# Optimization experiments

Hardware: AMD Instinct MI355X
Metric: run time of the kernel (lower is better)

## Reference

```python
import jax, jax.numpy as jnp
import numpy as np

N_NODES = 4096
N_EDGES = 131072
N_GRAPHS = 16
F_IN = 128
NUM_CLASSES = 10
NH = 4  # heads per MHA and number of MHA modules
D = 128  # embed dim after conv2
HD = D // NH  # 32 per-head dim


def setup_inputs() -> dict:
    key = jax.random.key(0)
    ks = jax.random.split(key, 20)
    p = lambda i, shape: jax.random.normal(ks[i], shape, dtype=jnp.float32) * 0.05
    return {
        "x": jax.random.normal(ks[0], (N_NODES, F_IN), dtype=jnp.float32),
        "edge_index": jax.random.randint(ks[1], (2, N_EDGES), 0, N_NODES, dtype=jnp.int32),
        "batch": jnp.sort(jax.random.randint(ks[2], (N_NODES,), 0, N_GRAPHS, dtype=jnp.int32)),
        # GCN layers (PyG GCNConv: lin without bias, bias added after aggregation)
        "W1": p(3, (64, F_IN)), "b1": p(4, (64,)),
        "W2": p(5, (128, 64)), "b2": p(6, (128,)),
        # 4 MultiheadAttention modules, params stacked on axis 0
        "W_in": p(7, (NH, 3 * D, D)), "b_in": p(8, (NH, 3 * D)),
        "W_out": p(9, (NH, D, D)), "b_out": p(10, (NH, D)),
        # MLP head
        "Wf1": p(11, (256, D * NH)), "bf1": p(12, (256,)),
        "Wf2": p(13, (NUM_CLASSES, 256)), "bf2": p(14, (NUM_CLASSES,)),
    }


def gcn_conv(x, src, dst, dinv, W, b):
    # x' = x @ W.T; out[i] = sum_{j->i} dinv[j]*dinv[i] * x'[j] + b  (self-loops in src/dst)
    h = x @ W.T
    norm = dinv[src] * dinv[dst]  # [E+N]
    msg = h[src] * norm[:, None]
    return jax.ops.segment_sum(msg, dst, num_segments=N_NODES) + b


def mha(x, W_in, b_in, W_out, b_out):
    # x: [N, D] treated as batch=1, seq=N (torch MHA self-attention)
    qkv = x @ W_in.T + b_in  # [N, 3D]
    q, k, v = jnp.split(qkv, 3, axis=-1)
    q = q.reshape(-1, NH, HD).transpose(1, 0, 2)  # [H, N, HD]
    k = k.reshape(-1, NH, HD).transpose(1, 0, 2)
    v = v.reshape(-1, NH, HD).transpose(1, 0, 2)
    scores = jnp.einsum("hnd,hmd->hnm", q, k) / jnp.sqrt(jnp.float32(HD))
    attn = jax.nn.softmax(scores, axis=-1)
    o = jnp.einsum("hnm,hmd->hnd", attn, v)  # [H, N, HD]
    o = o.transpose(1, 0, 2).reshape(-1, D)  # [N, D]
    return o @ W_out.T + b_out


def reference(x, edge_index, batch, W1, b1, W2, b2, W_in, b_in, W_out, b_out, Wf1, bf1, Wf2, bf2):
    # add self-loops (PyG GCNConv default)
    loop = jnp.arange(N_NODES, dtype=edge_index.dtype)
    src = jnp.concatenate([edge_index[0], loop])
    dst = jnp.concatenate([edge_index[1], loop])
    deg = jax.ops.segment_sum(jnp.ones_like(src, dtype=jnp.float32), dst, num_segments=N_NODES)
    dinv = jnp.where(deg > 0, jax.lax.rsqrt(jnp.maximum(deg, 1.0)), 0.0)

    h = jax.nn.relu(gcn_conv(x, src, dst, dinv, W1, b1))
    h = jax.nn.relu(gcn_conv(h, src, dst, dinv, W2, b2))

    # 4 independent MHA modules over the same node sequence, concatenated
    outs = jax.vmap(mha, in_axes=(None, 0, 0, 0, 0))(h, W_in, b_in, W_out, b_out)  # [4, N, D]
    h = outs.transpose(1, 0, 2).reshape(N_NODES, D * NH)  # [N, 512]

    # global mean pool per graph
    sums = jax.ops.segment_sum(h, batch, num_segments=N_GRAPHS)
    cnts = jax.ops.segment_sum(jnp.ones((N_NODES,), jnp.float32), batch, num_segments=N_GRAPHS)
    g = sums / jnp.maximum(cnts, 1.0)[:, None]  # [16, 512]

    g = jax.nn.relu(g @ Wf1.T + bf1)
    logits = g @ Wf2.T + bf2
    return jax.nn.log_softmax(logits, axis=1)
```

## Files before the change

### kernel.cpp

```cpp
#include <hip/hip_runtime.h>
#include <hip/hip_bf16.h>

#define N_NODES 4096
#define N_EDGES 131072
#define N_GRAPHS 16
#define F_IN 128
#define D 128
#define QKVLD 1536
#define KSPL 2
#define CHUNK 64
#define NT (2048 / CHUNK)

typedef __hip_bfloat16 bf16;
typedef __attribute__((ext_vector_type(4))) float f32x4;
typedef __attribute__((ext_vector_type(8))) short bf16x8;

__device__ __forceinline__ short f2bf(float f) {
    unsigned u = __float_as_uint(f);
    unsigned r = (u + 0x7fffu + ((u >> 16) & 1u)) >> 16;
    return (short)r;
}
__device__ __forceinline__ float bf2f(short b) {
    return __uint_as_float(((unsigned)(unsigned short)b) << 16);
}
__device__ __forceinline__ float ldf(const void* p, long i, int isbf) {
    return isbf ? bf2f(((const short*)p)[i]) : ((const float*)p)[i];
}
__device__ __forceinline__ int swzK(int a) { return a ^ (((a >> 7) & 3) << 4); }
__device__ __forceinline__ int swzV(int a) { return a ^ (((a >> 7) & 7) << 4); }

__global__ void k_detect(const void* __restrict__ x, int* __restrict__ flag) {
    if (threadIdx.x == 0 && blockIdx.x == 0) {
        const unsigned short* h = (const unsigned short*)x;
        int bf = 1;
        for (int i = 0; i < 64; ++i) {
            int e = (h[i] >> 7) & 0xFF;
            if (e >= 134) { bf = 0; break; }
        }
        *flag = bf;
    }
}

struct ConvSegs {
    const void* src0; const void* src1; const void* src2; const void* src3; const void* src4;
    short* dst0; short* dst1; short* dst2; short* dst3; short* dst4;
    int e0, e1, e2, e3, e4;
};
__global__ void k_tobf16(ConvSegs s, const int* __restrict__ flag) {
    int idx = blockIdx.x * 256 + threadIdx.x;
    int isbf = *flag;
    const void* src; short* dst; int base;
    if (idx < s.e0)      { src = s.src0; dst = s.dst0; base = 0; }
    else if (idx < s.e1) { src = s.src1; dst = s.dst1; base = s.e0; }
    else if (idx < s.e2) { src = s.src2; dst = s.dst2; base = s.e1; }
    else if (idx < s.e3) { src = s.src3; dst = s.dst3; base = s.e2; }
    else if (idx < s.e4) { src = s.src4; dst = s.dst4; base = s.e3; }
    else return;
    int i = idx - base;
    dst[i] = f2bf(ldf(src, i, isbf));
}

__global__ void k_deg(const int* __restrict__ dst, int* __restrict__ degi) {
    int e = blockIdx.x * 256 + threadIdx.x;
    if (e < N_EDGES) atomicAdd(&degi[dst[e]], 1);
}

__global__ __launch_bounds__(1024) void k_prep(const int* __restrict__ degi,
                                               const int* __restrict__ batch,
                                               int* __restrict__ offs,
                                               int* __restrict__ cursor,
                                               float* __restrict__ dinv,
                                               int* __restrict__ starts) {
    __shared__ int part[1024];
    int t = threadIdx.x;
    int4 v = *(const int4*)(degi + t * 4);
    int dv[4] = {v.x, v.y, v.z, v.w};
    int s = dv[0] + dv[1] + dv[2] + dv[3];
    part[t] = s;
    __syncthreads();
    for (int ofs = 1; ofs < 1024; ofs <<= 1) {
        int val = (t >= ofs) ? part[t - ofs] : 0;
        __syncthreads();
        part[t] += val;
        __syncthreads();
    }
    int o = part[t] - s;
#pragma unroll
    for (int j = 0; j < 4; ++j) {
        int n = t * 4 + j;
        offs[n] = o; cursor[n] = o;
        o += dv[j];
        dinv[n] = rsqrtf((float)(dv[j] + 1));
    }
    if (t == 1023) offs[4096] = o;
#pragma unroll
    for (int j = 0; j < 4; ++j) {
        int n = t * 4 + j;
        int b = batch[n];
        if (n == 0) { for (int g2 = 0; g2 <= b; ++g2) starts[g2] = 0; }
        else {
            int pb = batch[n - 1];
            for (int g2 = pb + 1; g2 <= b; ++g2) starts[g2] = n;
        }
        if (n == N_NODES - 1) { for (int g2 = b + 1; g2 <= N_GRAPHS; ++g2) starts[g2] = N_NODES; }
    }
}

__global__ void k_sortedges(const int* __restrict__ src, const int* __restrict__ dst,
                            int* __restrict__ cursor, int* __restrict__ sSrc) {
    int e = blockIdx.x * 256 + threadIdx.x;
    if (e >= N_EDGES) return;
    int d = dst[e];
    int pos = atomicAdd(&cursor[d], 1);
    sSrc[pos] = src[e];
}

__global__ __launch_bounds__(64) void k_mfma_gemm_s(const short* __restrict__ A, int lda,
                                                    const short* __restrict__ W,
                                                    short* __restrict__ C, int ldc, int K) {
    const int lane = threadIdx.x;
    const int m15 = lane & 15, quad = lane >> 4;
    const int c0 = blockIdx.x * 16;
    const int n0 = blockIdx.y * 16;
    f32x4 acc = {0.f, 0.f, 0.f, 0.f};
    for (int k0 = 0; k0 < K; k0 += 32) {
        bf16x8 a = *(const bf16x8*)(A + (long)(n0 + m15) * lda + k0 + quad * 8);
        bf16x8 b = *(const bf16x8*)(W + (long)(c0 + m15) * K + k0 + quad * 8);
        acc = __builtin_amdgcn_mfma_f32_16x16x32_bf16(a, b, acc, 0, 0, 0);
    }
#pragma unroll
    for (int i = 0; i < 4; ++i)
        C[(long)(n0 + quad * 4 + i) * ldc + c0 + m15] = f2bf(acc[i]);
}

__global__ __launch_bounds__(64) void k_qkv(const short* __restrict__ h2b,
                                            const short* __restrict__ Winb,
                                            const void* __restrict__ bin,
                                            const int* __restrict__ flag,
                                            short* __restrict__ Qb,
                                            short* __restrict__ Kb,
                                            short* __restrict__ VTb) {
    const int lane = threadIdx.x;
    const int m15 = lane & 15, quad = lane >> 4;
    const int c0 = blockIdx.x * 16;
    const int n0 = blockIdx.y * 16;
    f32x4 acc = {0.f, 0.f, 0.f, 0.f};
#pragma unroll
    for (int k0 = 0; k0 < 128; k0 += 32) {
        bf16x8 a = *(const bf16x8*)(h2b + (long)(n0 + m15) * 128 + k0 + quad * 8);
        bf16x8 b = *(const bf16x8*)(Winb + (long)(c0 + m15) * 128 + k0 + quad * 8);
        acc = __builtin_amdgcn_mfma_f32_16x16x32_bf16(a, b, acc, 0, 0, 0);
    }
    const int c = c0 + m15;
    const int mmod = c / 384;
    const int r = c - mmod * 384;
    const int sect = r >> 7;
    const int rr = r & 127;
    const int head = mmod * 4 + (rr >> 5);
    const int d = rr & 31;
    const float bias = ldf(bin, c, *flag);
    if (sect == 0) {
        const float scale = 0.17677669529663687f * 1.4426950408889634f;
#pragma unroll
        for (int i = 0; i < 4; ++i)
            Qb[(long)head * 131072 + (long)(n0 + quad * 4 + i) * 32 + d] = f2bf((acc[i] + bias) * scale);
    } else if (sect == 1) {
#pragma unroll
        for (int i = 0; i < 4; ++i)
            Kb[(long)head * 131072 + (long)(n0 + quad * 4 + i) * 32 + d] = f2bf(acc[i] + bias);
    } else {
        long vbase = (long)head * 131072 + (long)d * 4096;
#pragma unroll
        for (int i = 0; i < 4; ++i) {
            int n = n0 + quad * 4 + i;
            int phys = (n & ~31) | ((((n >> 2) & 3) << 3) | (((n >> 4) & 1) << 2) | (n & 3));
            VTb[vbase + phys] = f2bf(acc[i] + bias);
        }
    }
}

__global__ __launch_bounds__(64) void k_gather64(const short* __restrict__ hlin,
                                                 const int* __restrict__ offs,
                                                 const int* __restrict__ sSrc,
                                                 const float* __restrict__ dinv,
                                                 const void* __restrict__ bias,
                                                 const int* __restrict__ flag,
                                                 short* __restrict__ houtb) {
    int n = blockIdx.x;
    int c = threadIdx.x;
    int beg = offs[n], end = offs[n + 1];
    float di = dinv[n];
    float acc = 0.f;
    for (int j = beg; j < end; ++j) {
        int s = sSrc[j];
        acc += dinv[s] * bf2f(hlin[(long)s * 64 + c]);
    }
    float v = fmaxf(di * acc + di * di * bf2f(hlin[(long)n * 64 + c]) + ldf(bias, c, *flag), 0.f);
    houtb[(long)n * 64 + c] = f2bf(v);
}

__global__ __launch_bounds__(128) void k_gather128(const short* __restrict__ hlin,
                                                   const int* __restrict__ offs,
                                                   const int* __restrict__ sSrc,
                                                   const float* __restrict__ dinv,
                                                   const void* __restrict__ bias,
                                                   const int* __restrict__ flag,
                                                   short* __restrict__ h2b) {
    int n = blockIdx.x;
    int c = threadIdx.x;
    int beg = offs[n], end = offs[n + 1];
    float di = dinv[n];
    float acc = 0.f;
    for (int j = beg; j < end; ++j) {
        int s = sSrc[j];
        acc += dinv[s] * bf2f(hlin[(long)s * 128 + c]);
    }
    float v = fmaxf(di * acc + di * di * bf2f(hlin[(long)n * 128 + c]) + ldf(bias, c, *flag), 0.f);
    h2b[(long)n * 128 + c] = f2bf(v);
}

__global__ __launch_bounds__(512) void k_attn_v13(const short* __restrict__ Qb,
                                                  const short* __restrict__ Kb,
                                                  const short* __restrict__ VTb,
                                                  short* __restrict__ po_base,
                                                  float* __restrict__ pl) {
    const int tid = threadIdx.x;
    const int lane = tid & 63;
    const int wid = tid >> 6;
    const int m15 = lane & 15, quad = lane >> 4;
    const int b = blockIdx.x;
    const int mh = (b & 7) + 8 * (b >> 8);
    const int mid = (b >> 3) & 31;
    const int z = mid & 1;
    const int qb = mid >> 1;
    const int q0 = qb * 256 + wid * 32;
    const long hoff = (long)mh * 131072;
    const short* Qh = Qb + hoff;
    const short* Kh = Kb + hoff;
    const short* Vh = VTb + hoff;
    const int ks0 = z * 2048;

    __shared__ short Klds[2][2048];
    __shared__ short Vlds[2][2048];

    int myOff, dstB;
    if (tid < 256) {
        int r = tid >> 2, part = tid & 3;
        myOff = r * 32 + part * 8;
        dstB  = swzK(r * 64 + part * 16);
    } else {
        int u = tid - 256;
        int d = u >> 3, part = u & 7;
        myOff = d * 4096 + part * 8;
        dstB  = swzV(d * 128 + part * 16);
    }

    const bf16x8 qf0 = *(const bf16x8*)(Qh + (long)(q0 + m15) * 32 + quad * 8);
    const bf16x8 qf1 = *(const bf16x8*)(Qh + (long)(q0 + 16 + m15) * 32 + quad * 8);

    const int k00 = swzK((0 * 32 + m15) * 64 + quad * 16);
    const int k01 = swzK((0 * 32 + 16 + m15) * 64 + quad * 16);
    const int k10 = swzK((1 * 32 + m15) * 64 + quad * 16);
    const int k11 = swzK((1 * 32 + 16 + m15) * 64 + quad * 16);
    const int v00 = swzV(m15 * 128 + 0 * 64 + quad * 16);
    const int v01 = swzV((16 + m15) * 128 + 0 * 64 + quad * 16);
    const int v10 = swzV(m15 * 128 + 1 * 64 + quad * 16);
    const int v11 = swzV((16 + m15) * 128 + 1 * 64 + quad * 16);

    f32x4 oA0 = {0.f,0.f,0.f,0.f}, oA1 = {0.f,0.f,0.f,0.f};
    f32x4 oB0 = {0.f,0.f,0.f,0.f}, oB1 = {0.f,0.f,0.f,0.f};
    float lq0 = 0.f, lq1 = 0.f;

    int4 nx = (tid < 256) ? *(const int4*)(Kh + (long)ks0 * 32 + myOff)
                          : *(const int4*)(Vh + myOff + ks0);
    if (tid < 256) *(int4*)((char*)&Klds[0][0] + dstB) = nx;
    else           *(int4*)((char*)&Vlds[0][0] + dstB) = nx;
    __syncthreads();

    int cur = 0;
    for (int c = 0; c < NT; ++c) {
        const bool more = (c + 1 < NT);
        if (more) {
            int kc = ks0 + (c + 1) * CHUNK;
            nx = (tid < 256) ? *(const int4*)(Kh + (long)kc * 32 + myOff)
                             : *(const int4*)(Vh + myOff + kc);
        }
        const char* Kc = (const char*)&Klds[cur][0];
        const char* Vc = (const char*)&Vlds[cur][0];
#pragma unroll
        for (int s = 0; s < 2; ++s) {
            bf16x8 kf0 = *(const bf16x8*)(Kc + (s ? k10 : k00));
            bf16x8 kf1 = *(const bf16x8*)(Kc + (s ? k11 : k01));
            bf16x8 vf0 = *(const bf16x8*)(Vc + (s ? v10 : v00));
            bf16x8 vf1 = *(const bf16x8*)(Vc + (s ? v11 : v01));
            const f32x4 zz = {0.f,0.f,0.f,0.f};
            __builtin_amdgcn_s_setprio(1);
            f32x4 sA0 = __builtin_amdgcn_mfma_f32_16x16x32_bf16(kf0, qf0, zz, 0, 0, 0);
            f32x4 sA1 = __builtin_amdgcn_mfma_f32_16x16x32_bf16(kf1, qf0, zz, 0, 0, 0);
            f32x4 sB0 = __builtin_amdgcn_mfma_f32_16x16x32_bf16(kf0, qf1, zz, 0, 0, 0);
            f32x4 sB1 = __builtin_amdgcn_mfma_f32_16x16x32_bf16(kf1, qf1, zz, 0, 0, 0);
            __builtin_amdgcn_s_setprio(0);
            float pA0[4], pA1[4], pB0[4], pB1[4];
#pragma unroll
            for (int i = 0; i < 4; ++i) {
                pA0[i] = __builtin_amdgcn_exp2f(fminf(sA0[i], 100.f));
                pA1[i] = __builtin_amdgcn_exp2f(fminf(sA1[i], 100.f));
                pB0[i] = __builtin_amdgcn_exp2f(fminf(sB0[i], 100.f));
                pB1[i] = __builtin_amdgcn_exp2f(fminf(sB1[i], 100.f));
            }
            lq0 += (pA0[0] + pA0[1]) + (pA0[2] + pA0[3]) + (pA1[0] + pA1[1]) + (pA1[2] + pA1[3]);
            lq1 += (pB0[0] + pB0[1]) + (pB0[2] + pB0[3]) + (pB1[0] + pB1[1]) + (pB1[2] + pB1[3]);
            union { unsigned u[4]; bf16x8 v; } aq0, aq1;
            aq0.u[0] = __builtin_amdgcn_perm(__float_as_uint(pA0[1]), __float_as_uint(pA0[0]), 0x07060302u);
            aq0.u[1] = __builtin_amdgcn_perm(__float_as_uint(pA0[3]), __float_as_uint(pA0[2]), 0x07060302u);
            aq0.u[2] = __builtin_amdgcn_perm(__float_as_uint(pA1[1]), __float_as_uint(pA1[0]), 0x07060302u);
            aq0.u[3] = __builtin_amdgcn_perm(__float_as_uint(pA1[3]), __float_as_uint(pA1[2]), 0x07060302u);
            aq1.u[0] = __builtin_amdgcn_perm(__float_as_uint(pB0[1]), __float_as_uint(pB0[0]), 0x07060302u);
            aq1.u[1] = __builtin_amdgcn_perm(__float_as_uint(pB0[3]), __float_as_uint(pB0[2]), 0x07060302u);
            aq1.u[2] = __builtin_amdgcn_perm(__float_as_uint(pB1[1]), __float_as_uint(pB1[0]), 0x07060302u);
            aq1.u[3] = __builtin_amdgcn_perm(__float_as_uint(pB1[3]), __float_as_uint(pB1[2]), 0x07060302u);
            __builtin_amdgcn_s_setprio(1);
            oA0 = __builtin_amdgcn_mfma_f32_16x16x32_bf16(aq0.v, vf0, oA0, 0, 0, 0);
            oA1 = __builtin_amdgcn_mfma_f32_16x16x32_bf16(aq0.v, vf1, oA1, 0, 0, 0);
            oB0 = __builtin_amdgcn_mfma_f32_16x16x32_bf16(aq1.v, vf0, oB0, 0, 0, 0);
            oB1 = __builtin_amdgcn_mfma_f32_16x16x32_bf16(aq1.v, vf1, oB1, 0, 0, 0);
            __builtin_amdgcn_s_setprio(0);
        }
        if (more) {
            if (tid < 256) *(int4*)((char*)&Klds[cur ^ 1][0] + dstB) = nx;
            else           *(int4*)((char*)&Vlds[cur ^ 1][0] + dstB) = nx;
        }
        __syncthreads();
        cur ^= 1;
    }

    lq0 += __shfl_xor(lq0, 16); lq0 += __shfl_xor(lq0, 32);
    lq1 += __shfl_xor(lq1, 16); lq1 += __shfl_xor(lq1, 32);

    short* po = po_base + (long)z * 2097152;
    const int base = (mh >> 2) * 128 + (mh & 3) * 32;
#pragma unroll
    for (int i = 0; i < 4; ++i) {
        int qa = q0 + quad * 4 + i;
        int qb2 = qa + 16;
        po[(long)qa * 512 + base + m15]       = f2bf(oA0[i]);
        po[(long)qa * 512 + base + 16 + m15]  = f2bf(oA1[i]);
        po[(long)qb2 * 512 + base + m15]      = f2bf(oB0[i]);
        po[(long)qb2 * 512 + base + 16 + m15] = f2bf(oB1[i]);
    }
    if (quad == 0) {
        pl[z * 65536 + mh * 4096 + q0 + m15] = lq0;
        pl[z * 65536 + mh * 4096 + q0 + 16 + m15] = lq1;
    }
}

__global__ __launch_bounds__(64) void k_outproj(const short* __restrict__ po,
                                                const float* __restrict__ pl,
                                                const short* __restrict__ Woutb,
                                                const void* __restrict__ bout,
                                                const int* __restrict__ flag,
                                                float* __restrict__ hcat) {
    const int lane = threadIdx.x;
    const int m15 = lane & 15, quad = lane >> 4;
    const int c0 = blockIdx.x * 16;
    const int n0 = blockIdx.y * 16;
    const int m = blockIdx.z;
    const int n = n0 + m15;
    f32x4 acc = {0.f,0.f,0.f,0.f};
#pragma unroll
    for (int k0 = 0; k0 < 128; k0 += 32) {
        const int head = m * 4 + (k0 >> 5);
        float l = pl[head * 4096 + n] + pl[65536 + head * 4096 + n];
        float inv = 1.f / fmaxf(l, 1e-30f);
        long base = (long)n * 512 + m * 128 + k0 + quad * 8;
        bf16x8 a0 = *(const bf16x8*)(po + base);
        bf16x8 a1 = *(const bf16x8*)(po + 2097152 + base);
        bf16x8 av;
#pragma unroll
        for (int j = 0; j < 8; ++j)
            av[j] = f2bf((bf2f(a0[j]) + bf2f(a1[j])) * inv);
        bf16x8 bv = *(const bf16x8*)(Woutb + (long)(m * 128 + c0 + m15) * 128 + k0 + quad * 8);
        acc = __builtin_amdgcn_mfma_f32_16x16x32_bf16(av, bv, acc, 0, 0, 0);
    }
    float bias = ldf(bout, m * 128 + c0 + m15, *flag);
#pragma unroll
    for (int i = 0; i < 4; ++i)
        hcat[(long)(n0 + quad * 4 + i) * 512 + m * 128 + c0 + m15] = acc[i] + bias;
}

__global__ __launch_bounds__(1024) void k_pool3(const float* __restrict__ hcat,
                                                const int* __restrict__ starts,
                                                float* __restrict__ g) {
    int gr = blockIdx.x, cg = blockIdx.y;
    int tx = threadIdx.x, ty = threadIdx.y;
    int c = cg * 128 + tx;
    int beg = starts[gr], end = starts[gr + 1];
    float s = 0.f;
    for (int n = beg + ty; n < end; n += 8)
        s += hcat[(long)n * 512 + c];
    __shared__ float red[8][128];
    red[ty][tx] = s;
    __syncthreads();
    if (ty == 0) {
        float t = ((red[0][tx] + red[1][tx]) + (red[2][tx] + red[3][tx]))
                + ((red[4][tx] + red[5][tx]) + (red[6][tx] + red[7][tx]));
        int cnt = end - beg;
        g[gr * 512 + c] = t / (float)(cnt > 0 ? cnt : 1);
    }
}

__global__ void k_gemm_mlp(const float* __restrict__ A, int lda,
                           const void* __restrict__ W,
                           const void* __restrict__ bias,
                           const int* __restrict__ flag,
                           float* __restrict__ C, int ldc,
                           int M, int N, int K, int relu) {
    const int wb = *flag;
    __shared__ float As[16][17];
    __shared__ float Ws[16][17];
    int tx = threadIdx.x, ty = threadIdx.y;
    int row = blockIdx.y * 16 + ty;
    int col = blockIdx.x * 16 + tx;
    float acc = 0.f;
    for (int k0 = 0; k0 < K; k0 += 16) {
        As[ty][tx] = (row < M && (k0 + tx) < K) ? A[(long)row * lda + k0 + tx] : 0.f;
        int wrow = blockIdx.x * 16 + ty;
        Ws[ty][tx] = (wrow < N && (k0 + tx) < K) ? ldf(W, (long)wrow * K + k0 + tx, wb) : 0.f;
        __syncthreads();
#pragma unroll
        for (int kk = 0; kk < 16; ++kk) acc += As[ty][kk] * Ws[tx][kk];
        __syncthreads();
    }
    if (row < M && col < N) {
        if (bias) acc += ldf(bias, col, wb);
        if (relu) acc = fmaxf(acc, 0.f);
        C[(long)row * ldc + col] = acc;
    }
}

__global__ void k_logsoftmax(const float* __restrict__ logits, const int* __restrict__ flag,
                             void* __restrict__ out) {
    int t = threadIdx.x;
    if (t >= N_GRAPHS) return;
    int isbf = *flag;
    float v[10];
    float mx = -1e30f;
    for (int c = 0; c < 10; ++c) { v[c] = logits[t * 10 + c]; mx = fmaxf(mx, v[c]); }
    float s = 0.f;
    for (int c = 0; c < 10; ++c) s += __expf(v[c] - mx);
    float lse = mx + __logf(s);
    for (int c = 0; c < 10; ++c) {
        float r = v[c] - lse;
        if (isbf) ((bf16*)out)[t * 10 + c] = (bf16)r;
        else      ((float*)out)[t * 10 + c] = r;
    }
}

extern "C" void kernel_launch(void* const* d_in, const int* in_sizes, int n_in,
                              void* d_out, int out_size, void* d_ws, size_t ws_size,
                              hipStream_t stream) {
    const void* x     = d_in[0];
    const int*  ei    = (const int*)d_in[1];
    const int*  batch = (const int*)d_in[2];
    const void* W1    = d_in[3];
    const void* b1    = d_in[4];
    const void* W2    = d_in[5];
    const void* b2    = d_in[6];
    const void* W_in  = d_in[7];
    const void* b_in  = d_in[8];
    const void* W_out = d_in[9];
    const void* b_out = d_in[10];
    const void* Wf1   = d_in[11];
    const void* bf1   = d_in[12];
    const void* Wf2   = d_in[13];
    const void* bf2   = d_in[14];

    const int* src = ei;
    const int* dst = ei + N_EDGES;

    float* w = (float*)d_ws;
    size_t off = 0;
    auto alloc = [&](size_t n) { float* p = w + off; off += (n + 63) & ~(size_t)63; return p; };
    int*   flag   = (int*)alloc(64);
    float* dinv   = alloc(N_NODES);
    float* g      = alloc(N_GRAPHS * 512);
    float* hid    = alloc(N_GRAPHS * 256);
    float* logits = alloc(N_GRAPHS * 10);
    int*   degi   = (int*)alloc(N_NODES);
    int*   offs   = (int*)alloc(N_NODES + 64);
    int*   cursor = (int*)alloc(N_NODES);
    int*   sSrc   = (int*)alloc(N_EDGES);
    int*   starts = (int*)alloc(64);
    float* pl     = alloc(KSPL * 16 * N_NODES);
    float* xbf    = alloc(262144);
    float* W1bf   = alloc(4096);
    float* W2bf   = alloc(4096);
    float* Winbf  = alloc(98304);
    float* Woutbf = alloc(32768);
    float* h1linbf= alloc(131072);
    float* h2linbf= alloc(262144);
    float* h1bf   = alloc(131072);
    float* h2bf   = alloc(262144);
    float* pobf   = alloc((size_t)KSPL * 1048576);
    float* hcat   = alloc(2097152);
    float* bufQ   = alloc(3145728);

    short* xb    = (short*)xbf;
    short* W1b   = (short*)W1bf;
    short* W2b   = (short*)W2bf;
    short* Winb  = (short*)Winbf;
    short* Woutb = (short*)Woutbf;
    short* h1lin = (short*)h1linbf;
    short* h2lin = (short*)h2linbf;
    short* h1b   = (short*)h1bf;
    short* h2b   = (short*)h2bf;
    short* po    = (short*)pobf;
    short* Qb    = (short*)bufQ;
    short* Kb    = Qb + 2097152;
    short* VTb   = Qb + 4194304;

    dim3 b256(256);

    k_detect<<<dim3(1), dim3(64), 0, stream>>>(x, flag);

    ConvSegs cs;
    cs.src0 = x;     cs.dst0 = xb;    cs.e0 = 524288;
    cs.src1 = W1;    cs.dst1 = W1b;   cs.e1 = cs.e0 + 8192;
    cs.src2 = W2;    cs.dst2 = W2b;   cs.e2 = cs.e1 + 8192;
    cs.src3 = W_in;  cs.dst3 = Winb;  cs.e3 = cs.e2 + 196608;
    cs.src4 = W_out; cs.dst4 = Woutb; cs.e4 = cs.e3 + 65536;
    k_tobf16<<<dim3((802816 + 255) / 256), b256, 0, stream>>>(cs, flag);

    hipMemsetAsync(degi, 0, N_NODES * sizeof(int), stream);
    k_deg<<<dim3((N_EDGES + 255) / 256), b256, 0, stream>>>(dst, degi);
    k_prep<<<dim3(1), dim3(1024), 0, stream>>>(degi, batch, offs, cursor, dinv, starts);
    k_sortedges<<<dim3((N_EDGES + 255) / 256), b256, 0, stream>>>(src, dst, cursor, sSrc);

    k_mfma_gemm_s<<<dim3(4, N_NODES / 16), dim3(64), 0, stream>>>(
        xb, F_IN, W1b, h1lin, 64, F_IN);
    k_gather64<<<dim3(N_NODES), dim3(64), 0, stream>>>(h1lin, offs, sSrc, dinv, b1, flag, h1b);

    k_mfma_gemm_s<<<dim3(8, N_NODES / 16), dim3(64), 0, stream>>>(
        h1b, 64, W2b, h2lin, 128, 64);
    k_gather128<<<dim3(N_NODES), dim3(128), 0, stream>>>(h2lin, offs, sSrc, dinv, b2, flag, h2b);

    k_qkv<<<dim3(96, N_NODES / 16), dim3(64), 0, stream>>>(
        h2b, Winb, b_in, flag, Qb, Kb, VTb);

    k_attn_v13<<<dim3(512), dim3(512), 0, stream>>>(Qb, Kb, VTb, po, pl);

    k_outproj<<<dim3(8, N_NODES / 16, 4), dim3(64), 0, stream>>>(
        po, pl, Woutb, b_out, flag, hcat);

    k_pool3<<<dim3(N_GRAPHS, 4), dim3(128, 8), 0, stream>>>(hcat, starts, g);
    k_gemm_mlp<<<dim3(256 / 16, 1), dim3(16, 16), 0, stream>>>(
        g, 512, Wf1, bf1, flag, hid, 256, N_GRAPHS, 256, 512, 1);
    k_gemm_mlp<<<dim3(1, 1), dim3(16, 16), 0, stream>>>(
        hid, 256, Wf2, bf2, flag, logits, 10, N_GRAPHS, 10, 256, 0);
    k_logsoftmax<<<dim3(1), dim3(64), 0, stream>>>(logits, flag, d_out);
}
```

Baseline: 293.2 us.

## Double attention K/V chunk size and split normalization out of out-projection

The attention kernel now stages 128-key chunks of K and V in shared memory instead of 64, so every thread loads both a K and a V vector each step, and the V swizzle is adjusted for the wider row stride. This halves the number of barrier-separated iterations and spreads the load work across all threads, at the cost of twice the LDS footprint per block. The softmax-denominator normalization and the merge of the two key-split partials move out of the out-projection GEMM into a separate k_norm kernel. The out-projection previously redid that work for every column tile; the new kernel does it once, but adds a launch and an extra write and read of the normalized buffer.

```diff
diff --git a/kernel.cpp b/kernel.cpp
--- a/kernel.cpp
+++ b/kernel.cpp
@@ -8,7 +8,7 @@
 #define D 128
 #define QKVLD 1536
 #define KSPL 2
-#define CHUNK 64
+#define CHUNK 128
 #define NT (2048 / CHUNK)
 
 typedef __hip_bfloat16 bf16;
@@ -27,7 +27,7 @@
     return isbf ? bf2f(((const short*)p)[i]) : ((const float*)p)[i];
 }
 __device__ __forceinline__ int swzK(int a) { return a ^ (((a >> 7) & 3) << 4); }
-__device__ __forceinline__ int swzV(int a) { return a ^ (((a >> 7) & 7) << 4); }
+__device__ __forceinline__ int swzV(int a) { return a ^ (((a >> 8) & 7) << 4); }
 
 __global__ void k_detect(const void* __restrict__ x, int* __restrict__ flag) {
     if (threadIdx.x == 0 && blockIdx.x == 0) {
@@ -219,7 +219,7 @@
     h2b[(long)n * 128 + c] = f2bf(v);
 }
 
-__global__ __launch_bounds__(512) void k_attn_v13(const short* __restrict__ Qb,
+__global__ __launch_bounds__(512) void k_attn_v15(const short* __restrict__ Qb,
                                                   const short* __restrict__ Kb,
                                                   const short* __restrict__ VTb,
                                                   short* __restrict__ po_base,
@@ -240,41 +240,32 @@
     const short* Vh = VTb + hoff;
     const int ks0 = z * 2048;
 
-    __shared__ short Klds[2][2048];
-    __shared__ short Vlds[2][2048];
-
-    int myOff, dstB;
-    if (tid < 256) {
-        int r = tid >> 2, part = tid & 3;
-        myOff = r * 32 + part * 8;
-        dstB  = swzK(r * 64 + part * 16);
-    } else {
-        int u = tid - 256;
-        int d = u >> 3, part = u & 7;
-        myOff = d * 4096 + part * 8;
-        dstB  = swzV(d * 128 + part * 16);
-    }
+    __shared__ short Klds[2][4096];
+    __shared__ short Vlds[2][4096];
+
+    const int rK = tid >> 2, pK = tid & 3;
+    const int  offK = rK * 32 + pK * 8;
+    const int  dstK = swzK(rK * 64 + pK * 16);
+    const int dV = tid >> 4, pV = tid & 15;
+    const long offV = (long)dV * 4096 + pV * 8;
+    const int  dstV = swzV(dV * 256 + pV * 16);
 
     const bf16x8 qf0 = *(const bf16x8*)(Qh + (long)(q0 + m15) * 32 + quad * 8);
     const bf16x8 qf1 = *(const bf16x8*)(Qh + (long)(q0 + 16 + m15) * 32 + quad * 8);
 
-    const int k00 = swzK((0 * 32 + m15) * 64 + quad * 16);
-    const int k01 = swzK((0 * 32 + 16 + m15) * 64 + quad * 16);
-    const int k10 = swzK((1 * 32 + m15) * 64 + quad * 16);
-    const int k11 = swzK((1 * 32 + 16 + m15) * 64 + quad * 16);
-    const int v00 = swzV(m15 * 128 + 0 * 64 + quad * 16);
-    const int v01 = swzV((16 + m15) * 128 + 0 * 64 + quad * 16);
-    const int v10 = swzV(m15 * 128 + 1 * 64 + quad * 16);
-    const int v11 = swzV((16 + m15) * 128 + 1 * 64 + quad * 16);
+    const int kb0 = swzK(m15 * 64 + quad * 16);
+    const int kb1 = swzK((16 + m15) * 64 + quad * 16);
+    const int vb0 = swzV(m15 * 256 + quad * 16);
+    const int vb1 = swzV((16 + m15) * 256 + quad * 16);
 
     f32x4 oA0 = {0.f,0.f,0.f,0.f}, oA1 = {0.f,0.f,0.f,0.f};
     f32x4 oB0 = {0.f,0.f,0.f,0.f}, oB1 = {0.f,0.f,0.f,0.f};
     float lq0 = 0.f, lq1 = 0.f;
 
-    int4 nx = (tid < 256) ? *(const int4*)(Kh + (long)ks0 * 32 + myOff)
-                          : *(const int4*)(Vh + myOff + ks0);
-    if (tid < 256) *(int4*)((char*)&Klds[0][0] + dstB) = nx;
-    else           *(int4*)((char*)&Vlds[0][0] + dstB) = nx;
+    int4 nxK = *(const int4*)(Kh + (long)ks0 * 32 + offK);
+    int4 nxV = *(const int4*)(Vh + offV + ks0);
+    *(int4*)((char*)&Klds[0][0] + dstK) = nxK;
+    *(int4*)((char*)&Vlds[0][0] + dstV) = nxV;
     __syncthreads();
 
     int cur = 0;
@@ -282,17 +273,17 @@
         const bool more = (c + 1 < NT);
         if (more) {
             int kc = ks0 + (c + 1) * CHUNK;
-            nx = (tid < 256) ? *(const int4*)(Kh + (long)kc * 32 + myOff)
-                             : *(const int4*)(Vh + myOff + kc);
+            nxK = *(const int4*)(Kh + (long)kc * 32 + offK);
+            nxV = *(const int4*)(Vh + offV + kc);
         }
         const char* Kc = (const char*)&Klds[cur][0];
         const char* Vc = (const char*)&Vlds[cur][0];
 #pragma unroll
-        for (int s = 0; s < 2; ++s) {
-            bf16x8 kf0 = *(const bf16x8*)(Kc + (s ? k10 : k00));
-            bf16x8 kf1 = *(const bf16x8*)(Kc + (s ? k11 : k01));
-            bf16x8 vf0 = *(const bf16x8*)(Vc + (s ? v10 : v00));
-            bf16x8 vf1 = *(const bf16x8*)(Vc + (s ? v11 : v01));
+        for (int s = 0; s < 4; ++s) {
+            bf16x8 kf0 = *(const bf16x8*)(Kc + kb0 + s * 2048);
+            bf16x8 kf1 = *(const bf16x8*)(Kc + kb1 + s * 2048);
+            bf16x8 vf0 = *(const bf16x8*)(Vc + vb0 + s * 64);
+            bf16x8 vf1 = *(const bf16x8*)(Vc + vb1 + s * 64);
             const f32x4 zz = {0.f,0.f,0.f,0.f};
             __builtin_amdgcn_s_setprio(1);
             f32x4 sA0 = __builtin_amdgcn_mfma_f32_16x16x32_bf16(kf0, qf0, zz, 0, 0, 0);
@@ -327,8 +318,8 @@
             __builtin_amdgcn_s_setprio(0);
         }
         if (more) {
-            if (tid < 256) *(int4*)((char*)&Klds[cur ^ 1][0] + dstB) = nx;
-            else           *(int4*)((char*)&Vlds[cur ^ 1][0] + dstB) = nx;
+            *(int4*)((char*)&Klds[cur ^ 1][0] + dstK) = nxK;
+            *(int4*)((char*)&Vlds[cur ^ 1][0] + dstV) = nxV;
         }
         __syncthreads();
         cur ^= 1;
@@ -354,8 +345,26 @@
     }
 }
 
-__global__ __launch_bounds__(64) void k_outproj(const short* __restrict__ po,
-                                                const float* __restrict__ pl,
+__global__ __launch_bounds__(256) void k_norm(const short* __restrict__ po,
+                                              const float* __restrict__ pl,
+                                              short* __restrict__ poN) {
+    int idx = blockIdx.x * 256 + threadIdx.x;
+    int n = idx >> 6;
+    int col = (idx & 63) * 8;
+    int mh = ((col >> 7) << 2) | ((col >> 5) & 3);
+    float l = pl[mh * 4096 + n] + pl[65536 + mh * 4096 + n];
+    float inv = 1.f / fmaxf(l, 1e-30f);
+    long base = (long)n * 512 + col;
+    bf16x8 a0 = *(const bf16x8*)(po + base);
+    bf16x8 a1 = *(const bf16x8*)(po + 2097152 + base);
+    union { short s[8]; bf16x8 v; } r;
+#pragma unroll
+    for (int j = 0; j < 8; ++j)
+        r.s[j] = f2bf((bf2f(a0[j]) + bf2f(a1[j])) * inv);
+    *(bf16x8*)(poN + base) = r.v;
+}
+
+__global__ __launch_bounds__(64) void k_outproj(const short* __restrict__ poN,
                                                 const short* __restrict__ Woutb,
                                                 const void* __restrict__ bout,
                                                 const int* __restrict__ flag,
@@ -365,20 +374,10 @@
     const int c0 = blockIdx.x * 16;
     const int n0 = blockIdx.y * 16;
     const int m = blockIdx.z;
-    const int n = n0 + m15;
     f32x4 acc = {0.f,0.f,0.f,0.f};
 #pragma unroll
     for (int k0 = 0; k0 < 128; k0 += 32) {
-        const int head = m * 4 + (k0 >> 5);
-        float l = pl[head * 4096 + n] + pl[65536 + head * 4096 + n];
-        float inv = 1.f / fmaxf(l, 1e-30f);
-        long base = (long)n * 512 + m * 128 + k0 + quad * 8;
-        bf16x8 a0 = *(const bf16x8*)(po + base);
-        bf16x8 a1 = *(const bf16x8*)(po + 2097152 + base);
-        bf16x8 av;
-#pragma unroll
-        for (int j = 0; j < 8; ++j)
-            av[j] = f2bf((bf2f(a0[j]) + bf2f(a1[j])) * inv);
+        bf16x8 av = *(const bf16x8*)(poN + (long)(n0 + m15) * 512 + m * 128 + k0 + quad * 8);
         bf16x8 bv = *(const bf16x8*)(Woutb + (long)(m * 128 + c0 + m15) * 128 + k0 + quad * 8);
         acc = __builtin_amdgcn_mfma_f32_16x16x32_bf16(av, bv, acc, 0, 0, 0);
     }
@@ -502,6 +501,7 @@
     float* h1bf   = alloc(131072);
     float* h2bf   = alloc(262144);
     float* pobf   = alloc((size_t)KSPL * 1048576);
+    float* poNbf  = alloc(1048576);
     float* hcat   = alloc(2097152);
     float* bufQ   = alloc(3145728);
 
@@ -515,6 +515,7 @@
     short* h1b   = (short*)h1bf;
     short* h2b   = (short*)h2bf;
     short* po    = (short*)pobf;
+    short* poN   = (short*)poNbf;
     short* Qb    = (short*)bufQ;
     short* Kb    = Qb + 2097152;
     short* VTb   = Qb + 4194304;
@@ -547,10 +548,11 @@
     k_qkv<<<dim3(96, N_NODES / 16), dim3(64), 0, stream>>>(
         h2b, Winb, b_in, flag, Qb, Kb, VTb);
 
-    k_attn_v13<<<dim3(512), dim3(512), 0, stream>>>(Qb, Kb, VTb, po, pl);
-
+    k_attn_v15<<<dim3(512), dim3(512), 0, stream>>>(Qb, Kb, VTb, po, pl);
+
+    k_norm<<<dim3(1024), b256, 0, stream>>>(po, pl, poN);
     k_outproj<<<dim3(8, N_NODES / 16, 4), dim3(64), 0, stream>>>(
-        po, pl, Woutb, b_out, flag, hcat);
+        poN, Woutb, b_out, flag, hcat);
 
     k_pool3<<<dim3(N_GRAPHS, 4), dim3(128, 8), 0, stream>>>(hcat, starts, g);
     k_gemm_mlp<<<dim3(256 / 16, 1), dim3(16, 16), 0, stream>>>(
```

New measurement: 298.3 us. Within noise of the previous version (+1.7%).
